# Performance work log

Hardware: AMD Instinct MI355X
Metric: run time of the kernel (lower is better)

Reference implementation:

```python
import jax, jax.numpy as jnp
import numpy as np

NUM_HEADS = 4
GN_GROUPS = 32
EPS = 1e-5


def setup_inputs() -> dict:
    key = jax.random.key(0)
    ks = jax.random.split(key, 6)
    B, C, H, W = 4, 256, 64, 64
    return {
        "x": jax.random.normal(ks[0], (B, C, H, W), dtype=jnp.float32),
        "gn_w": jnp.ones((C,), dtype=jnp.float32),
        "gn_b": jnp.zeros((C,), dtype=jnp.float32),
        "qkv_w": jax.random.normal(ks[1], (3 * C, C), dtype=jnp.float32) * 0.05,
        "qkv_b": jax.random.normal(ks[2], (3 * C,), dtype=jnp.float32) * 0.02,
        "proj_w": jax.random.normal(ks[3], (C, C), dtype=jnp.float32) * 0.05,
        "proj_b": jax.random.normal(ks[4], (C,), dtype=jnp.float32) * 0.02,
    }


def reference(x, gn_w, gn_b, qkv_w, qkv_b, proj_w, proj_b):
    b, c, h, w = x.shape
    L = h * w
    xf = x.reshape(b, c, L)

    # GroupNorm32: normalize over (channels_per_group, length) in float32
    xg = xf.reshape(b, GN_GROUPS, (c // GN_GROUPS) * L).astype(jnp.float32)
    mean = xg.mean(axis=-1, keepdims=True)
    var = xg.var(axis=-1, keepdims=True)
    xn = ((xg - mean) * jax.lax.rsqrt(var + EPS)).reshape(b, c, L).astype(x.dtype)
    xn = xn * gn_w[:, None] + gn_b[:, None]

    # 1x1 Conv1d == channel matmul: [3C, C] @ [b, C, L]
    qkv = jnp.einsum('oc,bcl->bol', qkv_w, xn) + qkv_b[:, None]

    # QKVAttentionLegacy
    ch = c // NUM_HEADS
    qkv_h = qkv.reshape(b * NUM_HEADS, 3 * ch, L)
    q, k, v = qkv_h[:, :ch], qkv_h[:, ch:2 * ch], qkv_h[:, 2 * ch:]
    scale = 1.0 / np.sqrt(np.sqrt(ch)).astype(np.float32)
    weight = jnp.einsum('bct,bcs->bts', q * scale, k * scale)  # [b*H, L, L]
    weight = jax.nn.softmax(weight.astype(jnp.float32), axis=-1).astype(qkv.dtype)
    a = jnp.einsum('bts,bcs->bct', weight, v).reshape(b, c, L)

    h_out = jnp.einsum('oc,bcl->bol', proj_w, a) + proj_b[:, None]
    return (xf + h_out).reshape(b, c, h, w)
```

## Files before the change

kernel.cpp:

```cpp
#include <hip/hip_runtime.h>
#include <math.h>

#define L 4096
#define C 256

typedef __attribute__((ext_vector_type(8))) short bf16x8;
typedef __attribute__((ext_vector_type(4))) short s16x4;
typedef __attribute__((ext_vector_type(4))) float f32x4;
typedef __attribute__((ext_vector_type(4))) unsigned int u32x4;

static __device__ __forceinline__ short f2bf(float f) {
  union { float f; unsigned u; } x{f};
  unsigned r = (x.u + 0x7fffu + ((x.u >> 16) & 1u)) >> 16;
  return (short)r;
}
static __device__ __forceinline__ short truncbf(float f) {
  union { float f; unsigned u; } x{f};
  return (short)(x.u >> 16);
}
static __device__ __forceinline__ unsigned pack2(float a, float b) {
  return (unsigned)(unsigned short)f2bf(a) | ((unsigned)(unsigned short)f2bf(b) << 16);
}
static __device__ __forceinline__ void gload_lds16(const void* g, void* l) {
  __builtin_amdgcn_global_load_lds(
      (const __attribute__((address_space(1))) unsigned int*)g,
      (__attribute__((address_space(3))) unsigned int*)l, 16, 0, 0);
}

__global__ __launch_bounds__(256) void w2bf(const float* __restrict__ wa, int na,
                                            const float* __restrict__ wb, int nb,
                                            short* __restrict__ da, short* __restrict__ db) {
  int i = blockIdx.x * 256 + threadIdx.x;
  if (i < na) da[i] = f2bf(wa[i]);
  else if (i < na + nb) db[i - na] = f2bf(wb[i - na]);
}

__global__ __launch_bounds__(256) void gn_stats(const float* __restrict__ x,
                                                float* __restrict__ gnp) {
  int bg = blockIdx.x >> 2, q = blockIdx.x & 3;
  int tid = threadIdx.x;
  const f32x4* xp = (const f32x4*)(x + (size_t)bg * 32768 + (size_t)q * 8192);
  float s = 0.f, ss = 0.f;
  #pragma unroll
  for (int i = 0; i < 8; ++i) {
    f32x4 v = xp[i * 256 + tid];
    s  += v[0] + v[1] + v[2] + v[3];
    ss += v[0]*v[0] + v[1]*v[1] + v[2]*v[2] + v[3]*v[3];
  }
  __shared__ float rs[256], rss[256];
  rs[tid] = s; rss[tid] = ss;
  __syncthreads();
  for (int off = 128; off > 0; off >>= 1) {
    if (tid < off) { rs[tid] += rs[tid + off]; rss[tid] += rss[tid + off]; }
    __syncthreads();
  }
  if (tid == 0) {
    gnp[(size_t)blockIdx.x * 2]     = rs[0];
    gnp[(size_t)blockIdx.x * 2 + 1] = rss[0];
  }
}

__global__ __launch_bounds__(256) void gn_apply(const float* __restrict__ x,
    const float* __restrict__ gw, const float* __restrict__ gb,
    const float* __restrict__ gnp, short* __restrict__ xnT) {
  int bg = blockIdx.y;
  int b = bg >> 5, g = bg & 31;
  int tid = threadIdx.x;
  const float* xg = x + (size_t)bg * 32768;

  float s  = gnp[(size_t)(bg*4)*2]   + gnp[(size_t)(bg*4+1)*2] +
             gnp[(size_t)(bg*4+2)*2] + gnp[(size_t)(bg*4+3)*2];
  float ss = gnp[(size_t)(bg*4)*2+1]   + gnp[(size_t)(bg*4+1)*2+1] +
             gnp[(size_t)(bg*4+2)*2+1] + gnp[(size_t)(bg*4+3)*2+1];
  float mean = s * (1.f / 32768.f);
  float var  = ss * (1.f / 32768.f) - mean * mean;
  float rstd = rsqrtf(var + 1e-5f);

  float scl[8], sft[8];
  #pragma unroll
  for (int c = 0; c < 8; ++c) {
    float wv = gw[g * 8 + c], bv = gb[g * 8 + c];
    scl[c] = rstd * wv;
    sft[c] = bv - mean * rstd * wv;
  }

  short* outb = xnT + (size_t)b * L * C + g * 8;
  int lb = blockIdx.x * 1024 + tid * 4;
  f32x4 v[8];
  #pragma unroll
  for (int c = 0; c < 8; ++c)
    v[c] = *(const f32x4*)(xg + (size_t)c * L + lb);
  #pragma unroll
  for (int j = 0; j < 4; ++j) {
    u32x4 ov;
    #pragma unroll
    for (int cp = 0; cp < 4; ++cp)
      ov[cp] = pack2(v[2*cp][j]   * scl[2*cp]   + sft[2*cp],
                     v[2*cp+1][j] * scl[2*cp+1] + sft[2*cp+1]);
    *(u32x4*)(outb + (size_t)(lb + j) * C) = ov;
  }
}

__global__ __launch_bounds__(256) void qkv_mfma(const short* __restrict__ wq,
    const float* __restrict__ bias, const short* __restrict__ xnT,
    short* __restrict__ qT, short* __restrict__ kT, short* __restrict__ vB) {
  int tid = threadIdx.x;
  int wid = tid >> 6, lane = tid & 63, g = lane >> 4, lr = lane & 15;
  int oy = blockIdx.y;
  int o0 = oy * 64;
  int b  = blockIdx.z;
  int head = oy / 3, kind = oy % 3;
  int bh = b * 4 + head;
  int lw = blockIdx.x * 128 + wid * 32;
  const short* xb = xnT + (size_t)b * L * C;

  f32x4 acc[4][2];
  #pragma unroll
  for (int m = 0; m < 4; ++m)
    #pragma unroll
    for (int nt = 0; nt < 2; ++nt) acc[m][nt] = (f32x4)0.f;

  #pragma unroll 2
  for (int k0 = 0; k0 < C; k0 += 32) {
    bf16x8 af[4], bfr[2];
    #pragma unroll
    for (int m = 0; m < 4; ++m)
      af[m] = *(const bf16x8*)(wq + (size_t)(o0 + m * 16 + lr) * C + k0 + g * 8);
    #pragma unroll
    for (int nt = 0; nt < 2; ++nt)
      bfr[nt] = *(const bf16x8*)(xb + (size_t)(lw + nt * 16 + lr) * C + k0 + g * 8);
    #pragma unroll
    for (int m = 0; m < 4; ++m)
      #pragma unroll
      for (int nt = 0; nt < 2; ++nt)
        acc[m][nt] = __builtin_amdgcn_mfma_f32_16x16x32_bf16(af[m], bfr[nt], acc[m][nt], 0, 0, 0);
  }

  float sc = (kind == 0) ? 0.51014930f : (kind == 1) ? 0.35355339f : 1.0f;
  if (kind == 2) {
    #pragma unroll
    for (int m = 0; m < 4; ++m)
      #pragma unroll
      for (int nt = 0; nt < 2; ++nt)
        #pragma unroll
        for (int r = 0; r < 4; ++r) {
          int o = m * 16 + g * 4 + r;
          vB[((size_t)bh * 64 + o) * L + lw + nt * 16 + lr] =
              f2bf(acc[m][nt][r] + bias[o0 + o]);
        }
  } else {
    short* dst = (kind == 0 ? qT : kT);
    #pragma unroll
    for (int m = 0; m < 4; ++m)
      #pragma unroll
      for (int nt = 0; nt < 2; ++nt) {
        s16x4 pk;
        #pragma unroll
        for (int r = 0; r < 4; ++r)
          pk[r] = f2bf((acc[m][nt][r] + bias[o0 + m * 16 + g * 4 + r]) * sc);
        *(s16x4*)(dst + ((size_t)bh * L + lw + nt * 16 + lr) * 64 + m * 16 + g * 4) = pk;
      }
  }
}

__global__ __launch_bounds__(512) void attn_mfma(
    const short* __restrict__ qT, const short* __restrict__ kT,
    const short* __restrict__ vB, short* __restrict__ amatT) {
  int orig = blockIdx.x;
  int bid = (orig & 7) * 64 + (orig >> 3);
  int bh = bid >> 5, qb = bid & 31;
  int b = bh >> 2, h = bh & 3;
  int tid = threadIdx.x;
  int wid = tid >> 6, lane = tid & 63;
  int g = lane >> 4, lr = lane & 15;
  int tw = qb * 128 + wid * 16;
  int lx7 = lr & 7;
  int psw = (lr & 3) << 4;

  const short* qTh = qT + (size_t)bh * L * 64;
  const short* kTh = kT + (size_t)bh * L * 64;
  const short* vh  = vB + (size_t)bh * 64 * L;

  __shared__ short Kt[3][64 * 64];
  __shared__ short Vt[3][64 * 64];
  __shared__ short plds[8][16][72];

  bf16x8 qf[2];
  #pragma unroll
  for (int ks = 0; ks < 2; ++ks)
    qf[ks] = *(const bf16x8*)(qTh + (size_t)(tw + lr) * 64 + ks * 32 + g * 8);

  bf16x8 ones;
  #pragma unroll
  for (int i = 0; i < 8; ++i) ones[i] = (short)0x3F80;

  f32x4 acc[4], acc_l;
  #pragma unroll
  for (int cm = 0; cm < 4; ++cm) acc[cm] = (f32x4)0.f;
  acc_l = (f32x4)0.f;

  size_t koff, voff;
  int ldsc;
  {
    int r = tid >> 3, c16 = tid & 7;
    int cs = c16 ^ (r & 7);
    koff = (size_t)r * 64 + cs * 8;
    voff = (size_t)r * L + cs * 8;
    ldsc = wid * 512;
  }

  #define STAGE(buf, s0v)                                              \
    {                                                                  \
      gload_lds16(kTh + koff + (size_t)(s0v) * 64, &Kt[buf][ldsc]);    \
      gload_lds16(vh + voff + (size_t)(s0v), &Vt[buf][ldsc]);          \
    }

  auto compute = [&](const short* Kb, const short* Vb) {
    f32x4 st[4];
    __builtin_amdgcn_s_setprio(1);
    #pragma unroll
    for (int sm = 0; sm < 4; ++sm) {
      int row = sm * 16 + lr;
      bf16x8 kf0 = *(const bf16x8*)&Kb[row * 64 + ((0 * 4 + g) ^ lx7) * 8];
      bf16x8 kf1 = *(const bf16x8*)&Kb[row * 64 + ((1 * 4 + g) ^ lx7) * 8];
      f32x4 cc = (f32x4)0.f;
      cc = __builtin_amdgcn_mfma_f32_16x16x32_bf16(kf0, qf[0], cc, 0, 0, 0);
      cc = __builtin_amdgcn_mfma_f32_16x16x32_bf16(kf1, qf[1], cc, 0, 0, 0);
      st[sm] = cc;
    }
    __builtin_amdgcn_s_setprio(0);

    #pragma unroll
    for (int sm = 0; sm < 4; ++sm) {
      s16x4 pk;
      #pragma unroll
      for (int r = 0; r < 4; ++r)
        pk[r] = truncbf(__builtin_amdgcn_exp2f(st[sm][r]));
      *(s16x4*)&plds[wid][lr][(sm * 16 + g * 4) ^ psw] = pk;
    }

    bf16x8 pf[2];
    #pragma unroll
    for (int ks = 0; ks < 2; ++ks)
      pf[ks] = *(const bf16x8*)&plds[wid][lr][(ks * 32 + g * 8) ^ psw];
    __builtin_amdgcn_s_setprio(1);
    #pragma unroll
    for (int ks = 0; ks < 2; ++ks)
      acc_l = __builtin_amdgcn_mfma_f32_16x16x32_bf16(ones, pf[ks], acc_l, 0, 0, 0);
    #pragma unroll
    for (int cm = 0; cm < 4; ++cm) {
      int row = cm * 16 + lr;
      #pragma unroll
      for (int ks = 0; ks < 2; ++ks) {
        bf16x8 vf = *(const bf16x8*)&Vb[row * 64 + ((ks * 4 + g) ^ lx7) * 8];
        acc[cm] = __builtin_amdgcn_mfma_f32_16x16x32_bf16(vf, pf[ks], acc[cm], 0, 0, 0);
      }
    }
    __builtin_amdgcn_s_setprio(0);
  };

  STAGE(0, 0);
  STAGE(1, 64);
  asm volatile("s_waitcnt vmcnt(2)" ::: "memory");
  __builtin_amdgcn_s_barrier();
  __builtin_amdgcn_sched_barrier(0);

  int cur = 0, nxt = 2;
  #pragma unroll 1
  for (int t = 0; t < 62; ++t) {
    STAGE(nxt, (t + 2) * 64);
    compute(&Kt[cur][0], &Vt[cur][0]);
    asm volatile("s_waitcnt vmcnt(2)" ::: "memory");
    __builtin_amdgcn_s_barrier();
    __builtin_amdgcn_sched_barrier(0);
    cur = (cur == 2) ? 0 : cur + 1;
    nxt = (nxt == 2) ? 0 : nxt + 1;
  }
  compute(&Kt[cur][0], &Vt[cur][0]);
  asm volatile("s_waitcnt vmcnt(0)" ::: "memory");
  __builtin_amdgcn_s_barrier();
  __builtin_amdgcn_sched_barrier(0);
  cur = (cur == 2) ? 0 : cur + 1;
  compute(&Kt[cur][0], &Vt[cur][0]);

  float inv = 1.f / acc_l[0];
  #pragma unroll
  for (int cm = 0; cm < 4; ++cm) {
    s16x4 pk;
    #pragma unroll
    for (int r = 0; r < 4; ++r) pk[r] = f2bf(acc[cm][r] * inv);
    *(s16x4*)(amatT + ((size_t)b * L + tw + lr) * C + h * 64 + cm * 16 + g * 4) = pk;
  }
  #undef STAGE
}

__global__ __launch_bounds__(256) void proj_mfma(const short* __restrict__ pw,
    const float* __restrict__ bias, const short* __restrict__ amatT,
    const float* __restrict__ xres, float* __restrict__ out) {
  int tid = threadIdx.x;
  int wid = tid >> 6, lane = tid & 63, g = lane >> 4, lr = lane & 15;
  int o0 = blockIdx.y * 64;
  int b  = blockIdx.z;
  int lw = blockIdx.x * 128 + wid * 32;
  const short* ab = amatT + (size_t)b * L * C;

  f32x4 acc[4][2];
  #pragma unroll
  for (int m = 0; m < 4; ++m)
    #pragma unroll
    for (int nt = 0; nt < 2; ++nt) acc[m][nt] = (f32x4)0.f;

  #pragma unroll 2
  for (int k0 = 0; k0 < C; k0 += 32) {
    bf16x8 af[4], bfr[2];
    #pragma unroll
    for (int m = 0; m < 4; ++m)
      af[m] = *(const bf16x8*)(pw + (size_t)(o0 + m * 16 + lr) * C + k0 + g * 8);
    #pragma unroll
    for (int nt = 0; nt < 2; ++nt)
      bfr[nt] = *(const bf16x8*)(ab + (size_t)(lw + nt * 16 + lr) * C + k0 + g * 8);
    #pragma unroll
    for (int m = 0; m < 4; ++m)
      #pragma unroll
      for (int nt = 0; nt < 2; ++nt)
        acc[m][nt] = __builtin_amdgcn_mfma_f32_16x16x32_bf16(af[m], bfr[nt], acc[m][nt], 0, 0, 0);
  }

  #pragma unroll
  for (int m = 0; m < 4; ++m)
    #pragma unroll
    for (int nt = 0; nt < 2; ++nt)
      #pragma unroll
      for (int r = 0; r < 4; ++r) {
        int o = o0 + m * 16 + g * 4 + r;
        size_t idx = ((size_t)b * C + o) * L + lw + nt * 16 + lr;
        out[idx] = acc[m][nt][r] + bias[o] + xres[idx];
      }
}

extern "C" void kernel_launch(void* const* d_in, const int* in_sizes, int n_in,
                              void* d_out, int out_size, void* d_ws, size_t ws_size,
                              hipStream_t stream) {
  const float* x      = (const float*)d_in[0];
  const float* gn_w   = (const float*)d_in[1];
  const float* gn_b   = (const float*)d_in[2];
  const float* qkv_w  = (const float*)d_in[3];
  const float* qkv_b  = (const float*)d_in[4];
  const float* proj_w = (const float*)d_in[5];
  const float* proj_b = (const float*)d_in[6];
  float* out = (float*)d_out;

  short* xnT   = (short*)d_ws;
  short* qT    = xnT   + (size_t)4 * L * C;
  short* kT    = qT    + (size_t)16 * L * 64;
  short* vB    = kT    + (size_t)16 * L * 64;
  short* amatT = vB    + (size_t)16 * L * 64;
  short* wqbf  = amatT + (size_t)4 * L * C;
  short* pwbf  = wqbf  + (size_t)768 * C;
  float* gnp   = (float*)(pwbf + (size_t)C * C);

  w2bf<<<1024, 256, 0, stream>>>(qkv_w, 768 * C, proj_w, C * C, wqbf, pwbf);
  gn_stats<<<512, 256, 0, stream>>>(x, gnp);
  gn_apply<<<dim3(4, 128), 256, 0, stream>>>(x, gn_w, gn_b, gnp, xnT);
  qkv_mfma<<<dim3(32, 12, 4), 256, 0, stream>>>(wqbf, qkv_b, xnT, qT, kT, vB);
  attn_mfma<<<512, 512, 0, stream>>>(qT, kT, vB, amatT);
  proj_mfma<<<dim3(32, 4, 4), 256, 0, stream>>>(pwbf, proj_b, amatT, x, out);
}
```

Baseline: 157.3 us.

## Software-pipeline attention over paired key tiles and merge prep kernels

Restructures the attention main loop to process two 64-key tiles per iteration with four LDS buffers, loading the next pair while computing. The exp of one tile's scores is interleaved with the QK MFMAs of the next tile to overlap transcendental and matrix work. The P tile is packed with a perm-based truncation, and its LDS buffer is unpadded with a new XOR swizzle. The weight-conversion and GroupNorm-stats kernels are merged into one launch to save launch overhead, at the cost of more LDS and more register pressure.

After: 152.1 us. 3.3% less time.

```diff
diff --git a/kernel.cpp b/kernel.cpp
--- a/kernel.cpp
+++ b/kernel.cpp
@@ -7,19 +7,22 @@
 typedef __attribute__((ext_vector_type(8))) short bf16x8;
 typedef __attribute__((ext_vector_type(4))) short s16x4;
 typedef __attribute__((ext_vector_type(4))) float f32x4;
+typedef __attribute__((ext_vector_type(2))) unsigned int u32x2;
 typedef __attribute__((ext_vector_type(4))) unsigned int u32x4;
+
+#define MFMA16(a, b, c) __builtin_amdgcn_mfma_f32_16x16x32_bf16(a, b, c, 0, 0, 0)
 
 static __device__ __forceinline__ short f2bf(float f) {
   union { float f; unsigned u; } x{f};
   unsigned r = (x.u + 0x7fffu + ((x.u >> 16) & 1u)) >> 16;
   return (short)r;
 }
-static __device__ __forceinline__ short truncbf(float f) {
-  union { float f; unsigned u; } x{f};
-  return (short)(x.u >> 16);
-}
 static __device__ __forceinline__ unsigned pack2(float a, float b) {
   return (unsigned)(unsigned short)f2bf(a) | ((unsigned)(unsigned short)f2bf(b) << 16);
+}
+static __device__ __forceinline__ unsigned ppack(float a, float b) {
+  union { float f; unsigned u; } xa{a}, xb{b};
+  return __builtin_amdgcn_perm(xb.u, xa.u, 0x07060302u);
 }
 static __device__ __forceinline__ void gload_lds16(const void* g, void* l) {
   __builtin_amdgcn_global_load_lds(
@@ -27,36 +30,37 @@
       (__attribute__((address_space(3))) unsigned int*)l, 16, 0, 0);
 }
 
-__global__ __launch_bounds__(256) void w2bf(const float* __restrict__ wa, int na,
-                                            const float* __restrict__ wb, int nb,
-                                            short* __restrict__ da, short* __restrict__ db) {
-  int i = blockIdx.x * 256 + threadIdx.x;
-  if (i < na) da[i] = f2bf(wa[i]);
-  else if (i < na + nb) db[i - na] = f2bf(wb[i - na]);
-}
-
-__global__ __launch_bounds__(256) void gn_stats(const float* __restrict__ x,
-                                                float* __restrict__ gnp) {
-  int bg = blockIdx.x >> 2, q = blockIdx.x & 3;
-  int tid = threadIdx.x;
-  const f32x4* xp = (const f32x4*)(x + (size_t)bg * 32768 + (size_t)q * 8192);
-  float s = 0.f, ss = 0.f;
-  #pragma unroll
-  for (int i = 0; i < 8; ++i) {
-    f32x4 v = xp[i * 256 + tid];
-    s  += v[0] + v[1] + v[2] + v[3];
-    ss += v[0]*v[0] + v[1]*v[1] + v[2]*v[2] + v[3]*v[3];
-  }
-  __shared__ float rs[256], rss[256];
-  rs[tid] = s; rss[tid] = ss;
-  __syncthreads();
-  for (int off = 128; off > 0; off >>= 1) {
-    if (tid < off) { rs[tid] += rs[tid + off]; rss[tid] += rss[tid + off]; }
+__global__ __launch_bounds__(256) void prep(const float* __restrict__ x,
+    float* __restrict__ gnp, const float* __restrict__ wa,
+    const float* __restrict__ wb, short* __restrict__ da,
+    short* __restrict__ db) {
+  int blk = blockIdx.x;
+  int tid = threadIdx.x;
+  if (blk < 512) {
+    int bg = blk >> 2, q = blk & 3;
+    const f32x4* xp = (const f32x4*)(x + (size_t)bg * 32768 + (size_t)q * 8192);
+    float s = 0.f, ss = 0.f;
+    #pragma unroll
+    for (int i = 0; i < 8; ++i) {
+      f32x4 v = xp[i * 256 + tid];
+      s  += v[0] + v[1] + v[2] + v[3];
+      ss += v[0]*v[0] + v[1]*v[1] + v[2]*v[2] + v[3]*v[3];
+    }
+    __shared__ float rs[256], rss[256];
+    rs[tid] = s; rss[tid] = ss;
     __syncthreads();
-  }
-  if (tid == 0) {
-    gnp[(size_t)blockIdx.x * 2]     = rs[0];
-    gnp[(size_t)blockIdx.x * 2 + 1] = rss[0];
+    for (int off = 128; off > 0; off >>= 1) {
+      if (tid < off) { rs[tid] += rs[tid + off]; rss[tid] += rss[tid + off]; }
+      __syncthreads();
+    }
+    if (tid == 0) {
+      gnp[(size_t)blk * 2]     = rs[0];
+      gnp[(size_t)blk * 2 + 1] = rss[0];
+    }
+  } else {
+    int i = (blk - 512) * 256 + tid;
+    if (i < 768 * C) da[i] = f2bf(wa[i]);
+    else db[i - 768 * C] = f2bf(wb[i - 768 * C]);
   }
 }
 
@@ -133,7 +137,7 @@
     for (int m = 0; m < 4; ++m)
       #pragma unroll
       for (int nt = 0; nt < 2; ++nt)
-        acc[m][nt] = __builtin_amdgcn_mfma_f32_16x16x32_bf16(af[m], bfr[nt], acc[m][nt], 0, 0, 0);
+        acc[m][nt] = MFMA16(af[m], bfr[nt], acc[m][nt]);
   }
 
   float sc = (kind == 0) ? 0.51014930f : (kind == 1) ? 0.35355339f : 1.0f;
@@ -175,15 +179,15 @@
   int g = lane >> 4, lr = lane & 15;
   int tw = qb * 128 + wid * 16;
   int lx7 = lr & 7;
-  int psw = (lr & 3) << 4;
+  int pswA = ((lr & 3) << 4) | ((lr >> 2) << 2);
 
   const short* qTh = qT + (size_t)bh * L * 64;
   const short* kTh = kT + (size_t)bh * L * 64;
   const short* vh  = vB + (size_t)bh * 64 * L;
 
-  __shared__ short Kt[3][64 * 64];
-  __shared__ short Vt[3][64 * 64];
-  __shared__ short plds[8][16][72];
+  __shared__ short Kt[4][64 * 64];
+  __shared__ short Vt[4][64 * 64];
+  __shared__ short plds[8][16][64];
 
   bf16x8 qf[2];
   #pragma unroll
@@ -209,79 +213,105 @@
     ldsc = wid * 512;
   }
 
-  #define STAGE(buf, s0v)                                              \
-    {                                                                  \
-      gload_lds16(kTh + koff + (size_t)(s0v) * 64, &Kt[buf][ldsc]);    \
-      gload_lds16(vh + voff + (size_t)(s0v), &Vt[buf][ldsc]);          \
-    }
-
-  auto compute = [&](const short* Kb, const short* Vb) {
-    f32x4 st[4];
+  gload_lds16(kTh + koff, &Kt[0][ldsc]);
+  gload_lds16(vh + voff, &Vt[0][ldsc]);
+  gload_lds16(kTh + koff + (size_t)64 * 64, &Kt[1][ldsc]);
+  gload_lds16(vh + voff + 64, &Vt[1][ldsc]);
+
+  int sl = 0;
+  #pragma unroll 1
+  for (int s = 0; s < 32; ++s) {
+    if (s < 31) {
+      int nb = sl ^ 2;
+      size_t t0 = (size_t)(2 * s + 2) * 64, t1 = (size_t)(2 * s + 3) * 64;
+      gload_lds16(kTh + koff + t0 * 64, &Kt[nb][ldsc]);
+      gload_lds16(vh + voff + t0, &Vt[nb][ldsc]);
+      gload_lds16(kTh + koff + t1 * 64, &Kt[nb + 1][ldsc]);
+      gload_lds16(vh + voff + t1, &Vt[nb + 1][ldsc]);
+      asm volatile("s_waitcnt vmcnt(4)" ::: "memory");
+    } else {
+      asm volatile("s_waitcnt vmcnt(0)" ::: "memory");
+    }
+    __builtin_amdgcn_sched_barrier(0);
+    __builtin_amdgcn_s_barrier();
+
+    const short* Ka = &Kt[sl][0];     const short* Va = &Vt[sl][0];
+    const short* Kb = &Kt[sl + 1][0]; const short* Vb = &Vt[sl + 1][0];
+
+    f32x4 st0[4], st1[4];
     __builtin_amdgcn_s_setprio(1);
     #pragma unroll
     for (int sm = 0; sm < 4; ++sm) {
       int row = sm * 16 + lr;
-      bf16x8 kf0 = *(const bf16x8*)&Kb[row * 64 + ((0 * 4 + g) ^ lx7) * 8];
-      bf16x8 kf1 = *(const bf16x8*)&Kb[row * 64 + ((1 * 4 + g) ^ lx7) * 8];
+      bf16x8 kf0 = *(const bf16x8*)&Ka[row * 64 + (g ^ lx7) * 8];
+      bf16x8 kf1 = *(const bf16x8*)&Ka[row * 64 + ((4 + g) ^ lx7) * 8];
       f32x4 cc = (f32x4)0.f;
-      cc = __builtin_amdgcn_mfma_f32_16x16x32_bf16(kf0, qf[0], cc, 0, 0, 0);
-      cc = __builtin_amdgcn_mfma_f32_16x16x32_bf16(kf1, qf[1], cc, 0, 0, 0);
-      st[sm] = cc;
+      cc = MFMA16(kf0, qf[0], cc);
+      cc = MFMA16(kf1, qf[1], cc);
+      st0[sm] = cc;
     }
     __builtin_amdgcn_s_setprio(0);
-
     #pragma unroll
     for (int sm = 0; sm < 4; ++sm) {
-      s16x4 pk;
-      #pragma unroll
-      for (int r = 0; r < 4; ++r)
-        pk[r] = truncbf(__builtin_amdgcn_exp2f(st[sm][r]));
-      *(s16x4*)&plds[wid][lr][(sm * 16 + g * 4) ^ psw] = pk;
-    }
-
-    bf16x8 pf[2];
-    #pragma unroll
-    for (int ks = 0; ks < 2; ++ks)
-      pf[ks] = *(const bf16x8*)&plds[wid][lr][(ks * 32 + g * 8) ^ psw];
-    __builtin_amdgcn_s_setprio(1);
-    #pragma unroll
-    for (int ks = 0; ks < 2; ++ks)
-      acc_l = __builtin_amdgcn_mfma_f32_16x16x32_bf16(ones, pf[ks], acc_l, 0, 0, 0);
+      int row = sm * 16 + lr;
+      bf16x8 kf0 = *(const bf16x8*)&Kb[row * 64 + (g ^ lx7) * 8];
+      bf16x8 kf1 = *(const bf16x8*)&Kb[row * 64 + ((4 + g) ^ lx7) * 8];
+      f32x4 cc = (f32x4)0.f;
+      cc = MFMA16(kf0, qf[0], cc);
+      cc = MFMA16(kf1, qf[1], cc);
+      st1[sm] = cc;
+      u32x2 w;
+      w[0] = ppack(__builtin_amdgcn_exp2f(st0[sm][0]),
+                   __builtin_amdgcn_exp2f(st0[sm][1]));
+      w[1] = ppack(__builtin_amdgcn_exp2f(st0[sm][2]),
+                   __builtin_amdgcn_exp2f(st0[sm][3]));
+      *(u32x2*)&plds[wid][lr][(sm * 16 + g * 4) ^ pswA] = w;
+    }
+    bf16x8 pf0[2];
+    #pragma unroll
+    for (int ks = 0; ks < 2; ++ks) {
+      s16x4 pa = *(const s16x4*)&plds[wid][lr][(ks * 32 + g * 8) ^ pswA];
+      s16x4 pb = *(const s16x4*)&plds[wid][lr][(ks * 32 + g * 8 + 4) ^ pswA];
+      pf0[ks] = __builtin_shufflevector(pa, pb, 0, 1, 2, 3, 4, 5, 6, 7);
+    }
+    acc_l = MFMA16(ones, pf0[0], acc_l);
+    acc_l = MFMA16(ones, pf0[1], acc_l);
     #pragma unroll
     for (int cm = 0; cm < 4; ++cm) {
       int row = cm * 16 + lr;
-      #pragma unroll
-      for (int ks = 0; ks < 2; ++ks) {
-        bf16x8 vf = *(const bf16x8*)&Vb[row * 64 + ((ks * 4 + g) ^ lx7) * 8];
-        acc[cm] = __builtin_amdgcn_mfma_f32_16x16x32_bf16(vf, pf[ks], acc[cm], 0, 0, 0);
-      }
+      bf16x8 vf0 = *(const bf16x8*)&Va[row * 64 + (g ^ lx7) * 8];
+      bf16x8 vf1 = *(const bf16x8*)&Va[row * 64 + ((4 + g) ^ lx7) * 8];
+      acc[cm] = MFMA16(vf0, pf0[0], acc[cm]);
+      acc[cm] = MFMA16(vf1, pf0[1], acc[cm]);
+      u32x2 w;
+      w[0] = ppack(__builtin_amdgcn_exp2f(st1[cm][0]),
+                   __builtin_amdgcn_exp2f(st1[cm][1]));
+      w[1] = ppack(__builtin_amdgcn_exp2f(st1[cm][2]),
+                   __builtin_amdgcn_exp2f(st1[cm][3]));
+      *(u32x2*)&plds[wid][lr][(cm * 16 + g * 4) ^ pswA] = w;
+    }
+    bf16x8 pf1[2];
+    #pragma unroll
+    for (int ks = 0; ks < 2; ++ks) {
+      s16x4 pa = *(const s16x4*)&plds[wid][lr][(ks * 32 + g * 8) ^ pswA];
+      s16x4 pb = *(const s16x4*)&plds[wid][lr][(ks * 32 + g * 8 + 4) ^ pswA];
+      pf1[ks] = __builtin_shufflevector(pa, pb, 0, 1, 2, 3, 4, 5, 6, 7);
+    }
+    __builtin_amdgcn_s_setprio(1);
+    acc_l = MFMA16(ones, pf1[0], acc_l);
+    acc_l = MFMA16(ones, pf1[1], acc_l);
+    #pragma unroll
+    for (int cm = 0; cm < 4; ++cm) {
+      int row = cm * 16 + lr;
+      bf16x8 vf0 = *(const bf16x8*)&Vb[row * 64 + (g ^ lx7) * 8];
+      bf16x8 vf1 = *(const bf16x8*)&Vb[row * 64 + ((4 + g) ^ lx7) * 8];
+      acc[cm] = MFMA16(vf0, pf1[0], acc[cm]);
+      acc[cm] = MFMA16(vf1, pf1[1], acc[cm]);
     }
     __builtin_amdgcn_s_setprio(0);
-  };
-
-  STAGE(0, 0);
-  STAGE(1, 64);
-  asm volatile("s_waitcnt vmcnt(2)" ::: "memory");
-  __builtin_amdgcn_s_barrier();
-  __builtin_amdgcn_sched_barrier(0);
-
-  int cur = 0, nxt = 2;
-  #pragma unroll 1
-  for (int t = 0; t < 62; ++t) {
-    STAGE(nxt, (t + 2) * 64);
-    compute(&Kt[cur][0], &Vt[cur][0]);
-    asm volatile("s_waitcnt vmcnt(2)" ::: "memory");
     __builtin_amdgcn_s_barrier();
-    __builtin_amdgcn_sched_barrier(0);
-    cur = (cur == 2) ? 0 : cur + 1;
-    nxt = (nxt == 2) ? 0 : nxt + 1;
-  }
-  compute(&Kt[cur][0], &Vt[cur][0]);
-  asm volatile("s_waitcnt vmcnt(0)" ::: "memory");
-  __builtin_amdgcn_s_barrier();
-  __builtin_amdgcn_sched_barrier(0);
-  cur = (cur == 2) ? 0 : cur + 1;
-  compute(&Kt[cur][0], &Vt[cur][0]);
+    sl ^= 2;
+  }
 
   float inv = 1.f / acc_l[0];
   #pragma unroll
@@ -291,7 +321,6 @@
     for (int r = 0; r < 4; ++r) pk[r] = f2bf(acc[cm][r] * inv);
     *(s16x4*)(amatT + ((size_t)b * L + tw + lr) * C + h * 64 + cm * 16 + g * 4) = pk;
   }
-  #undef STAGE
 }
 
 __global__ __launch_bounds__(256) void proj_mfma(const short* __restrict__ pw,
@@ -323,7 +352,7 @@
     for (int m = 0; m < 4; ++m)
       #pragma unroll
       for (int nt = 0; nt < 2; ++nt)
-        acc[m][nt] = __builtin_amdgcn_mfma_f32_16x16x32_bf16(af[m], bfr[nt], acc[m][nt], 0, 0, 0);
+        acc[m][nt] = MFMA16(af[m], bfr[nt], acc[m][nt]);
   }
 
   #pragma unroll
@@ -359,8 +388,7 @@
   short* pwbf  = wqbf  + (size_t)768 * C;
   float* gnp   = (float*)(pwbf + (size_t)C * C);
 
-  w2bf<<<1024, 256, 0, stream>>>(qkv_w, 768 * C, proj_w, C * C, wqbf, pwbf);
-  gn_stats<<<512, 256, 0, stream>>>(x, gnp);
+  prep<<<1536, 256, 0, stream>>>(x, gnp, qkv_w, proj_w, wqbf, pwbf);
   gn_apply<<<dim3(4, 128), 256, 0, stream>>>(x, gn_w, gn_b, gnp, xnT);
   qkv_mfma<<<dim3(32, 12, 4), 256, 0, stream>>>(wqbf, qkv_b, xnT, qT, kT, vB);
   attn_mfma<<<512, 512, 0, stream>>>(qT, kT, vB, amatT);
```
